# Kernel tuning notes

Hardware: AMD Instinct MI355X
Metric: run time of the kernel (lower is better)

The kernel has to match this reference:

```python
import jax, jax.numpy as jnp
import numpy as np

B, N, D = 2048, 256, 2
HID = 256
MU, SIGMA = 0.1, 0.2  # concrete drift/diffusion for the abstract SDE: dX = mu*X dt + sigma*X dW


def _init_lin(key, fan_in, fan_out):
    return jax.random.normal(key, (fan_in, fan_out), dtype=jnp.float32) / np.sqrt(fan_in)


def setup_inputs() -> dict:
    key = jax.random.key(0)
    ks = jax.random.split(key, 8)
    ts = jnp.linspace(0.0, 1.0, N, dtype=jnp.float32)
    x0 = jax.random.normal(ks[0], (B, D), dtype=jnp.float32)
    eps = jax.random.normal(ks[1], (B, N, D), dtype=jnp.float32)  # raw unit gaussians
    return {
        "ts": ts, "x0": x0, "eps": eps,
        "fW0": _init_lin(ks[2], D + 1, HID), "fb0": jnp.zeros((HID,), jnp.float32),
        "fW1": _init_lin(ks[3], HID, HID), "fb1": jnp.zeros((HID,), jnp.float32),
        "fW2": _init_lin(ks[4], HID, 1), "fb2": jnp.zeros((1,), jnp.float32),
        "gW0": _init_lin(ks[5], D + 1, HID), "gb0": jnp.zeros((HID,), jnp.float32),
        "gW1": _init_lin(ks[6], HID, HID), "gb1": jnp.zeros((HID,), jnp.float32),
        "gW2": _init_lin(ks[7], HID, D), "gb2": jnp.zeros((D,), jnp.float32),
    }


def _mlp(tx, params):
    h = tx
    n = len(params)
    for i, (W, b) in enumerate(params):
        h = h @ W + b
        if i < n - 1:
            h = jax.nn.relu(h)
    return h


def _final(x):
    # concrete terminal condition g(X_T) = ||X_T||^2 (BaseFinal stand-in)
    return jnp.sum(x * x, axis=-1, keepdims=True)


def reference(ts, x0, eps, fW0, fb0, fW1, fb1, fW2, fb2, gW0, gb0, gW1, gb1, gW2, gb2):
    dt = ts[1:] - ts[:-1]                                  # (N-1,)
    dW = eps[:, : N - 1, :] * jnp.sqrt(dt)[None, :, None]  # (B, N-1, D) scaled increments

    def step(x, inp):
        dw_t, h = inp                                      # dw_t: (B,D), h: scalar
        x_new = x + MU * x * h + SIGMA * x * dw_t
        return x_new, x_new

    _, traj = jax.lax.scan(step, x0, (jnp.transpose(dW, (1, 0, 2)), dt))
    x = jnp.concatenate([x0[:, None, :], jnp.transpose(traj, (1, 0, 2))], axis=1)  # (B,N,D)
    # last increment slot is never filled in the torch loop -> zeros
    dW_full = jnp.concatenate([dW, jnp.zeros((B, 1, D), dW.dtype)], axis=1)        # (B,N,D)

    final_value = _final(x[:, -1, :])                      # (B,1)
    t = jnp.broadcast_to(ts[None, :, None], (B, N, 1))
    tx = jnp.concatenate([t, x], axis=2)                   # (B,N,D+1)

    Y = _mlp(tx, [(fW0, fb0), (fW1, fb1), (fW2, fb2)])     # (B,N,1)
    Z = _mlp(tx, [(gW0, gb0), (gW1, gb1), (gW2, gb2)])     # (B,N,D)

    # per-step targets: Y_{t+1} detached, final_value at the last step
    targets = jnp.concatenate(
        [jax.lax.stop_gradient(Y[:, 1:, :]), final_value[:, None, :]], axis=1)
    preds = Y + jnp.sum(Z * dW_full, axis=2, keepdims=True)  # (B,N,1)
    # sum over time of per-step MSE (mean over batch)
    loss = jnp.sum(jnp.mean((preds - targets) ** 2, axis=(0, 2)))
    return loss, Y, final_value
```

## Files before the change

kernel.cpp:

```cpp
#include <hip/hip_runtime.h>
#include <math.h>

#define B_ 2048
#define N_ 256
#define R_ (B_*N_)
#define MU_ 0.1f
#define SIGMA_ 0.2f
#define TILE_M 64
#define GRID_MLP 512
#define ITERS (R_ / TILE_M / GRID_MLP)

typedef __attribute__((ext_vector_type(4))) float f32x4;
typedef __attribute__((ext_vector_type(4))) int   i32x4;
typedef __attribute__((ext_vector_type(8))) int   i32x8;

__global__ void prep_weights(const float* __restrict__ fW1, const float* __restrict__ gW1,
                             unsigned int* __restrict__ wswz) {
    int idx = blockIdx.x * 256 + threadIdx.x;
    if (idx >= 2 * 16384) return;
    int m = idx >> 14, wi = idx & 16383;
    int frag = wi >> 9;
    int lane = (wi >> 3) & 63, q = wi & 7;
    int ki = frag >> 4, ct = frag & 15;
    int k = ki * 128 + (lane >> 4) * 32 + q * 4;
    int c = ct * 16 + (lane & 15);
    const float* W = m ? gW1 : fW1;
    float v0 = W[(k + 0) * 256 + c];
    float v1 = W[(k + 1) * 256 + c];
    float v2 = W[(k + 2) * 256 + c];
    float v3 = W[(k + 3) * 256 + c];
    int u = __builtin_amdgcn_cvt_pk_fp8_f32(v0, v1, 0, false);
    u = __builtin_amdgcn_cvt_pk_fp8_f32(v2, v3, u, true);
    wswz[idx] = (unsigned int)u;
}

__global__ void traj_kernel(const float* __restrict__ ts, const float* __restrict__ x0,
                            const float* __restrict__ eps, float* __restrict__ xs,
                            float* __restrict__ fv) {
    int gid = blockIdx.x * 256 + threadIdx.x;
    int b = gid >> 6, lane = gid & 63;
    int n0 = lane * 4;

    float t0 = ts[n0], t1 = ts[n0 + 1], t2 = ts[n0 + 2], t3 = ts[n0 + 3];
    float t4 = (n0 + 4 < N_) ? ts[n0 + 4] : t3;
    float h0 = t1 - t0, h1 = t2 - t1, h2 = t3 - t2, h3 = t4 - t3;
    float s0 = sqrtf(h0), s1 = sqrtf(h1), s2 = sqrtf(h2), s3 = sqrtf(h3);

    const float4* e4 = (const float4*)(eps + (size_t)(b * N_ + n0) * 2);
    float4 ea = e4[0], eb = e4[1];
    float f0a = 1.f + MU_ * h0 + SIGMA_ * (ea.x * s0);
    float f0b = 1.f + MU_ * h0 + SIGMA_ * (ea.y * s0);
    float f1a = 1.f + MU_ * h1 + SIGMA_ * (ea.z * s1);
    float f1b = 1.f + MU_ * h1 + SIGMA_ * (ea.w * s1);
    float f2a = 1.f + MU_ * h2 + SIGMA_ * (eb.x * s2);
    float f2b = 1.f + MU_ * h2 + SIGMA_ * (eb.y * s2);
    float f3a = 1.f + MU_ * h3 + SIGMA_ * (eb.z * s3);
    float f3b = 1.f + MU_ * h3 + SIGMA_ * (eb.w * s3);

    float Pa = f0a * f1a * f2a * f3a;
    float Pb = f0b * f1b * f2b * f3b;
    float Sa = Pa, Sb = Pb;
#pragma unroll
    for (int d = 1; d < 64; d <<= 1) {
        float va = __shfl_up(Sa, d);
        float vb = __shfl_up(Sb, d);
        if (lane >= d) { Sa *= va; Sb *= vb; }
    }
    float Ea = __shfl_up(Sa, 1);
    float Eb = __shfl_up(Sb, 1);
    if (lane == 0) { Ea = 1.f; Eb = 1.f; }

    float x0a = x0[2 * b], x0b = x0[2 * b + 1];
    float xa0 = x0a * Ea, xb0 = x0b * Eb;
    float xa1 = xa0 * f0a, xb1 = xb0 * f0b;
    float xa2 = xa1 * f1a, xb2 = xb1 * f1b;
    float xa3 = xa2 * f2a, xb3 = xb2 * f2b;

    float4* xsv = (float4*)(xs + (size_t)(b * N_ + n0) * 2);
    xsv[0] = make_float4(xa0, xb0, xa1, xb1);
    xsv[1] = make_float4(xa2, xb2, xa3, xb3);
    if (lane == 63) fv[b] = xa3 * xa3 + xb3 * xb3;
}

__global__ __launch_bounds__(512) void mlp_kernel(
        const float* __restrict__ ts, const float* __restrict__ eps, const float* __restrict__ xs,
        const unsigned int* __restrict__ wswz,
        const float* __restrict__ fW0, const float* __restrict__ fb0,
        const float* __restrict__ fb1, const float* __restrict__ fW2, const float* __restrict__ fb2,
        const float* __restrict__ gW0, const float* __restrict__ gb0,
        const float* __restrict__ gb1, const float* __restrict__ gW2, const float* __restrict__ gb2,
        float* __restrict__ Yout, float* __restrict__ zdot) {

    __shared__ __align__(16) unsigned char h0s[2][TILE_M * 256];
    __shared__ float st[TILE_M * ITERS], sx1[TILE_M * ITERS], sx2[TILE_M * ITERS];
    __shared__ float sd0[TILE_M * ITERS], sd1[TILE_M * ITERS];
    __shared__ float red[2][8][TILE_M];

    const int MLP = blockIdx.x & 1;
    const int bid = blockIdx.x >> 1;

    const float* W0 = MLP ? gW0 : fW0;
    const float* b0 = MLP ? gb0 : fb0;
    const float* b1 = MLP ? gb1 : fb1;
    const float* W2 = MLP ? gW2 : fW2;
    const float* b2 = MLP ? gb2 : fb2;
    float* outp     = MLP ? zdot : Yout;

    const int tid  = threadIdx.x;
    const int lane = tid & 63;
    const int w    = tid >> 6;
    const int arow = lane & 15;
    const int rg   = lane >> 4;

    const int c0 = (tid & 63) * 4;
    const int row0 = (tid >> 6) * 8;
    f32x4 w0t = *(const f32x4*)(W0 + c0);
    f32x4 w0x = *(const f32x4*)(W0 + 256 + c0);
    f32x4 w0y = *(const f32x4*)(W0 + 512 + c0);
    f32x4 w0bv = *(const f32x4*)(b0 + c0);

    f32x4 bi0 = *(const f32x4*)(b1 + w * 32 + 4 * rg);
    f32x4 bi1 = *(const f32x4*)(b1 + w * 32 + 16 + 4 * rg);
    f32x4 w20v[2], w21v[2];
#pragma unroll
    for (int p = 0; p < 2; ++p) {
        int c = w * 32 + p * 16 + 4 * rg;
        if (MLP) {
            f32x4 lo = *(const f32x4*)(W2 + 2 * c);
            f32x4 hi = *(const f32x4*)(W2 + 2 * c + 4);
            w20v[p] = (f32x4){lo[0], lo[2], hi[0], hi[2]};
            w21v[p] = (f32x4){lo[1], lo[3], hi[1], hi[3]};
        } else {
            w20v[p] = *(const f32x4*)(W2 + c);
            w21v[p] = (f32x4){0.f, 0.f, 0.f, 0.f};
        }
    }
    const float b20 = b2[0];
    const float b21 = MLP ? b2[1] : 0.f;

    i32x8 afrag[2][2];
    {
        const i32x4* wsw4 = (const i32x4*)(wswz + MLP * 16384);
#pragma unroll
        for (int ki = 0; ki < 2; ++ki)
#pragma unroll
            for (int p = 0; p < 2; ++p) {
                int base = ((ki * 16 + (w * 2 + p)) * 64 + lane) * 2;
                i32x4 lo = wsw4[base], hi = wsw4[base + 1];
                afrag[ki][p] = __builtin_shufflevector(lo, hi, 0, 1, 2, 3, 4, 5, 6, 7);
            }
    }

#pragma unroll
    for (int q = 0; q < 2; ++q) {
        int s = q * 512 + tid;
        int it = s >> 6, i = s & 63;
        int r = (bid + it * GRID_MLP) * TILE_M + i;
        int n = r & (N_ - 1);
        float2 xv = ((const float2*)xs)[r];
        float tv = ts[n];
        st[s] = tv; sx1[s] = xv.x; sx2[s] = xv.y;
        if (MLP) {
            float sdt = (n < N_ - 1) ? sqrtf(ts[n + 1] - tv) : 0.f;
            float2 ev = ((const float2*)eps)[r];
            sd0[s] = ev.x * sdt; sd1[s] = ev.y * sdt;
        }
    }
    __syncthreads();

#pragma unroll
    for (int ii = 0; ii < 8; ++ii) {
        int r = row0 + ii;
        float t = st[r], x1 = sx1[r], x2 = sx2[r];
        f32x4 h;
#pragma unroll
        for (int j = 0; j < 4; ++j)
            h[j] = fmaxf(fmaf(t, w0t[j], fmaf(x1, w0x[j], fmaf(x2, w0y[j], w0bv[j]))), 0.f);
        int q = __builtin_amdgcn_cvt_pk_fp8_f32(h[0], h[1], 0, false);
        q = __builtin_amdgcn_cvt_pk_fp8_f32(h[2], h[3], q, true);
        int off = r * 256 + (c0 ^ ((r & 7) << 5));
        *(unsigned int*)(h0s[0] + off) = (unsigned int)q;
    }
    __syncthreads();

    for (int t = 0; t < ITERS; ++t) {
        const int sb = t & 1;

        if (t > 0 && tid < TILE_M) {
            const int pb = sb ^ 1;
            float s = red[pb][0][tid] + red[pb][1][tid] + red[pb][2][tid] + red[pb][3][tid]
                    + red[pb][4][tid] + red[pb][5][tid] + red[pb][6][tid] + red[pb][7][tid];
            if (!MLP) s += b20;
            outp[(bid + (t - 1) * GRID_MLP) * TILE_M + tid] = s;
        }

        f32x4 acc[4][2];
#pragma unroll
        for (int rt = 0; rt < 4; ++rt) { acc[rt][0] = bi0; acc[rt][1] = bi1; }
#pragma unroll
        for (int ki = 0; ki < 2; ++ki) {
#pragma unroll
            for (int rt = 0; rt < 4; ++rt) {
                int row = rt * 16 + arow;
                int roff = row * 256 + ((ki * 128 + rg * 32) ^ ((row & 7) << 5));
                i32x4 blo = *(const i32x4*)(h0s[sb] + roff);
                i32x4 bhi = *(const i32x4*)(h0s[sb] + roff + 16);
                i32x8 bf = __builtin_shufflevector(blo, bhi, 0, 1, 2, 3, 4, 5, 6, 7);
                acc[rt][0] = __builtin_amdgcn_mfma_scale_f32_16x16x128_f8f6f4(
                                 afrag[ki][0], bf, acc[rt][0], 0, 0, 0, 127, 0, 127);
                acc[rt][1] = __builtin_amdgcn_mfma_scale_f32_16x16x128_f8f6f4(
                                 afrag[ki][1], bf, acc[rt][1], 0, 0, 0, 127, 0, 127);
            }
        }

#pragma unroll
        for (int rt = 0; rt < 4; ++rt) {
            float A0 = 0.f, A1 = 0.f;
#pragma unroll
            for (int p = 0; p < 2; ++p) {
#pragma unroll
                for (int i = 0; i < 4; ++i) {
                    float v = fmaxf(acc[rt][p][i], 0.f);
                    A0 = fmaf(v, w20v[p][i], A0);
                    if (MLP) A1 = fmaf(v, w21v[p][i], A1);
                }
            }
            A0 += __shfl_xor(A0, 16); A0 += __shfl_xor(A0, 32);
            if (MLP) { A1 += __shfl_xor(A1, 16); A1 += __shfl_xor(A1, 32); }
            if (rg == 0) {
                int row = rt * 16 + arow;
                float rv;
                if (MLP) {
                    int s = t * TILE_M + row;
                    float d0 = sd0[s], d1 = sd1[s];
                    rv = fmaf(A1, d1, A0 * d0);
                    if (w == 0) rv += fmaf(b21, d1, b20 * d0);
                } else {
                    rv = A0;
                }
                red[sb][w][row] = rv;
            }
        }

        if (t + 1 < ITERS) {
            const int sbase = (t + 1) * TILE_M;
#pragma unroll
            for (int ii = 0; ii < 8; ++ii) {
                int r = row0 + ii;
                int s = sbase + r;
                float tv = st[s], x1 = sx1[s], x2 = sx2[s];
                f32x4 h;
#pragma unroll
                for (int j = 0; j < 4; ++j)
                    h[j] = fmaxf(fmaf(tv, w0t[j], fmaf(x1, w0x[j], fmaf(x2, w0y[j], w0bv[j]))), 0.f);
                int q = __builtin_amdgcn_cvt_pk_fp8_f32(h[0], h[1], 0, false);
                q = __builtin_amdgcn_cvt_pk_fp8_f32(h[2], h[3], q, true);
                int off = r * 256 + (c0 ^ ((r & 7) << 5));
                *(unsigned int*)(h0s[sb ^ 1] + off) = (unsigned int)q;
            }
        }
        __syncthreads();
    }
    if (tid < TILE_M) {
        const int pb = (ITERS - 1) & 1;
        float s = red[pb][0][tid] + red[pb][1][tid] + red[pb][2][tid] + red[pb][3][tid]
                + red[pb][4][tid] + red[pb][5][tid] + red[pb][6][tid] + red[pb][7][tid];
        if (!MLP) s += b20;
        outp[(bid + (ITERS - 1) * GRID_MLP) * TILE_M + tid] = s;
    }
}

__global__ void loss_partial_kernel(const float* __restrict__ Yout, const float* __restrict__ fv,
                                    const float* __restrict__ zdot, float* __restrict__ partials) {
    __shared__ float wred[4];
    int tid = threadIdx.x;
    float s = 0.f;
    for (int r = blockIdx.x * 256 + tid; r < R_; r += gridDim.x * 256) {
        int n = r & (N_ - 1);
        float pred = Yout[r] + zdot[r];
        float target = (n == N_ - 1) ? fv[r >> 8] : Yout[r + 1];
        float d = pred - target;
        s = fmaf(d, d, s);
    }
#pragma unroll
    for (int m = 1; m < 64; m <<= 1) s += __shfl_xor(s, m);
    if ((tid & 63) == 0) wred[tid >> 6] = s;
    __syncthreads();
    if (tid == 0) partials[blockIdx.x] = wred[0] + wred[1] + wred[2] + wred[3];
}

__global__ void loss_final_kernel(const float* __restrict__ partials, float* __restrict__ out) {
    __shared__ float wred[4];
    int tid = threadIdx.x;
    float s = partials[tid] + partials[256 + tid] + partials[512 + tid] + partials[768 + tid];
#pragma unroll
    for (int m = 1; m < 64; m <<= 1) s += __shfl_xor(s, m);
    if ((tid & 63) == 0) wred[tid >> 6] = s;
    __syncthreads();
    if (tid == 0) out[0] = (wred[0] + wred[1] + wred[2] + wred[3]) * (1.0f / B_);
}

extern "C" void kernel_launch(void* const* d_in, const int* in_sizes, int n_in,
                              void* d_out, int out_size, void* d_ws, size_t ws_size,
                              hipStream_t stream) {
    const float* ts  = (const float*)d_in[0];
    const float* x0  = (const float*)d_in[1];
    const float* eps = (const float*)d_in[2];
    const float* fW0 = (const float*)d_in[3];
    const float* fb0 = (const float*)d_in[4];
    const float* fW1 = (const float*)d_in[5];
    const float* fb1 = (const float*)d_in[6];
    const float* fW2 = (const float*)d_in[7];
    const float* fb2 = (const float*)d_in[8];
    const float* gW0 = (const float*)d_in[9];
    const float* gb0 = (const float*)d_in[10];
    const float* gW1 = (const float*)d_in[11];
    const float* gb1 = (const float*)d_in[12];
    const float* gW2 = (const float*)d_in[13];
    const float* gb2 = (const float*)d_in[14];

    float* out  = (float*)d_out;
    float* Yout = out + 1;
    float* fv   = out + 1 + R_;

    char* wsb = (char*)d_ws;
    float* xs           = (float*)wsb;
    unsigned int* wswz  = (unsigned int*)(wsb + (4 << 20));
    float* zdot         = (float*)(wsb + (4 << 20) + (256 << 10));
    float* partials     = (float*)(wsb + (4 << 20) + (256 << 10) + (2 << 20));

    hipLaunchKernelGGL(prep_weights, dim3(128), dim3(256), 0, stream, fW1, gW1, wswz);
    hipLaunchKernelGGL(traj_kernel, dim3(512), dim3(256), 0, stream, ts, x0, eps, xs, fv);
    hipLaunchKernelGGL(mlp_kernel, dim3(2 * GRID_MLP), dim3(512), 0, stream,
                       ts, eps, xs, wswz,
                       fW0, fb0, fb1, fW2, fb2,
                       gW0, gb0, gb1, gW2, gb2, Yout, zdot);
    hipLaunchKernelGGL(loss_partial_kernel, dim3(1024), dim3(256), 0, stream, Yout, fv, zdot, partials);
    hipLaunchKernelGGL(loss_final_kernel, dim3(1), dim3(256), 0, stream, partials, out);
}
```

Measured before the change: 174.8 us.

## Rework MLP kernel LDS layout: 8-byte swizzle, packed inputs, shuffle-free reduction

Changes the fp8 activation tile swizzle to an 8-byte granularity XOR over 16 rows and reads B fragments as four 8-byte LDS loads, aiming to reduce bank conflicts. Packs the t/x and dW staging arrays into float4/float2 structs so each row is fetched in one vector load. Replaces the cross-lane shuffle reduction with per-lane partial writes into a padded 32-wide reduction buffer that is summed with vector reads. Adds s_setprio around the MFMA loop. The trade-offs are more LDS instructions per fragment and a larger reduction buffer, which may affect occupancy.

```diff
diff --git a/kernel.cpp b/kernel.cpp
--- a/kernel.cpp
+++ b/kernel.cpp
@@ -11,7 +11,7 @@
 #define ITERS (R_ / TILE_M / GRID_MLP)
 
 typedef __attribute__((ext_vector_type(4))) float f32x4;
-typedef __attribute__((ext_vector_type(4))) int   i32x4;
+typedef __attribute__((ext_vector_type(2))) int   i32x2;
 typedef __attribute__((ext_vector_type(8))) int   i32x8;
 
 __global__ void prep_weights(const float* __restrict__ fW1, const float* __restrict__ gW1,
@@ -92,9 +92,9 @@
         float* __restrict__ Yout, float* __restrict__ zdot) {
 
     __shared__ __align__(16) unsigned char h0s[2][TILE_M * 256];
-    __shared__ float st[TILE_M * ITERS], sx1[TILE_M * ITERS], sx2[TILE_M * ITERS];
-    __shared__ float sd0[TILE_M * ITERS], sd1[TILE_M * ITERS];
-    __shared__ float red[2][8][TILE_M];
+    __shared__ __align__(16) float4 sfx[TILE_M * ITERS];
+    __shared__ __align__(16) float2 sd[TILE_M * ITERS];
+    __shared__ __align__(16) float red2[2][TILE_M][36];
 
     const int MLP = blockIdx.x & 1;
     const int bid = blockIdx.x >> 1;
@@ -140,14 +140,14 @@
 
     i32x8 afrag[2][2];
     {
-        const i32x4* wsw4 = (const i32x4*)(wswz + MLP * 16384);
+        const i32x2* wsw2 = (const i32x2*)(wswz + MLP * 16384);
 #pragma unroll
         for (int ki = 0; ki < 2; ++ki)
 #pragma unroll
             for (int p = 0; p < 2; ++p) {
-                int base = ((ki * 16 + (w * 2 + p)) * 64 + lane) * 2;
-                i32x4 lo = wsw4[base], hi = wsw4[base + 1];
-                afrag[ki][p] = __builtin_shufflevector(lo, hi, 0, 1, 2, 3, 4, 5, 6, 7);
+                int base = ((ki * 16 + (w * 2 + p)) * 64 + lane) * 4;
+                i32x2 a0 = wsw2[base], a1 = wsw2[base + 1], a2 = wsw2[base + 2], a3 = wsw2[base + 3];
+                afrag[ki][p] = (i32x8){a0[0], a0[1], a1[0], a1[1], a2[0], a2[1], a3[0], a3[1]};
             }
     }
 
@@ -159,11 +159,11 @@
         int n = r & (N_ - 1);
         float2 xv = ((const float2*)xs)[r];
         float tv = ts[n];
-        st[s] = tv; sx1[s] = xv.x; sx2[s] = xv.y;
+        sfx[s] = make_float4(tv, xv.x, xv.y, 0.f);
         if (MLP) {
             float sdt = (n < N_ - 1) ? sqrtf(ts[n + 1] - tv) : 0.f;
             float2 ev = ((const float2*)eps)[r];
-            sd0[s] = ev.x * sdt; sd1[s] = ev.y * sdt;
+            sd[s] = make_float2(ev.x * sdt, ev.y * sdt);
         }
     }
     __syncthreads();
@@ -171,14 +171,14 @@
 #pragma unroll
     for (int ii = 0; ii < 8; ++ii) {
         int r = row0 + ii;
-        float t = st[r], x1 = sx1[r], x2 = sx2[r];
+        float4 v = sfx[r];
         f32x4 h;
 #pragma unroll
         for (int j = 0; j < 4; ++j)
-            h[j] = fmaxf(fmaf(t, w0t[j], fmaf(x1, w0x[j], fmaf(x2, w0y[j], w0bv[j]))), 0.f);
+            h[j] = fmaxf(fmaf(v.x, w0t[j], fmaf(v.y, w0x[j], fmaf(v.z, w0y[j], w0bv[j]))), 0.f);
         int q = __builtin_amdgcn_cvt_pk_fp8_f32(h[0], h[1], 0, false);
         q = __builtin_amdgcn_cvt_pk_fp8_f32(h[2], h[3], q, true);
-        int off = r * 256 + (c0 ^ ((r & 7) << 5));
+        int off = r * 256 + (c0 ^ ((r & 15) << 3));
         *(unsigned int*)(h0s[0] + off) = (unsigned int)q;
     }
     __syncthreads();
@@ -188,8 +188,13 @@
 
         if (t > 0 && tid < TILE_M) {
             const int pb = sb ^ 1;
-            float s = red[pb][0][tid] + red[pb][1][tid] + red[pb][2][tid] + red[pb][3][tid]
-                    + red[pb][4][tid] + red[pb][5][tid] + red[pb][6][tid] + red[pb][7][tid];
+            const float* rr = red2[pb][tid];
+            float s = 0.f;
+#pragma unroll
+            for (int j = 0; j < 32; j += 4) {
+                f32x4 v = *(const f32x4*)(rr + j);
+                s += (v[0] + v[1]) + (v[2] + v[3]);
+            }
             if (!MLP) s += b20;
             outp[(bid + (t - 1) * GRID_MLP) * TILE_M + tid] = s;
         }
@@ -197,21 +202,27 @@
         f32x4 acc[4][2];
 #pragma unroll
         for (int rt = 0; rt < 4; ++rt) { acc[rt][0] = bi0; acc[rt][1] = bi1; }
+        __builtin_amdgcn_s_setprio(1);
 #pragma unroll
         for (int ki = 0; ki < 2; ++ki) {
 #pragma unroll
             for (int rt = 0; rt < 4; ++rt) {
                 int row = rt * 16 + arow;
-                int roff = row * 256 + ((ki * 128 + rg * 32) ^ ((row & 7) << 5));
-                i32x4 blo = *(const i32x4*)(h0s[sb] + roff);
-                i32x4 bhi = *(const i32x4*)(h0s[sb] + roff + 16);
-                i32x8 bf = __builtin_shufflevector(blo, bhi, 0, 1, 2, 3, 4, 5, 6, 7);
+                const int rsw = (row & 15) << 3;
+                const unsigned char* bp = h0s[sb] + row * 256;
+                const int kb = ki * 128 + rg * 32;
+                i32x2 q0 = *(const i32x2*)(bp + ((kb +  0) ^ rsw));
+                i32x2 q1 = *(const i32x2*)(bp + ((kb +  8) ^ rsw));
+                i32x2 q2 = *(const i32x2*)(bp + ((kb + 16) ^ rsw));
+                i32x2 q3 = *(const i32x2*)(bp + ((kb + 24) ^ rsw));
+                i32x8 bf = (i32x8){q0[0], q0[1], q1[0], q1[1], q2[0], q2[1], q3[0], q3[1]};
                 acc[rt][0] = __builtin_amdgcn_mfma_scale_f32_16x16x128_f8f6f4(
                                  afrag[ki][0], bf, acc[rt][0], 0, 0, 0, 127, 0, 127);
                 acc[rt][1] = __builtin_amdgcn_mfma_scale_f32_16x16x128_f8f6f4(
                                  afrag[ki][1], bf, acc[rt][1], 0, 0, 0, 127, 0, 127);
             }
         }
+        __builtin_amdgcn_s_setprio(0);
 
 #pragma unroll
         for (int rt = 0; rt < 4; ++rt) {
@@ -225,21 +236,16 @@
                     if (MLP) A1 = fmaf(v, w21v[p][i], A1);
                 }
             }
-            A0 += __shfl_xor(A0, 16); A0 += __shfl_xor(A0, 32);
-            if (MLP) { A1 += __shfl_xor(A1, 16); A1 += __shfl_xor(A1, 32); }
-            if (rg == 0) {
-                int row = rt * 16 + arow;
-                float rv;
-                if (MLP) {
-                    int s = t * TILE_M + row;
-                    float d0 = sd0[s], d1 = sd1[s];
-                    rv = fmaf(A1, d1, A0 * d0);
-                    if (w == 0) rv += fmaf(b21, d1, b20 * d0);
-                } else {
-                    rv = A0;
-                }
-                red[sb][w][row] = rv;
-            }
+            int row = rt * 16 + arow;
+            float rv;
+            if (MLP) {
+                float2 dv = sd[t * TILE_M + row];
+                rv = fmaf(A1, dv.y, A0 * dv.x);
+                if (w == 0) rv += fmaf(b21, dv.y, b20 * dv.x);
+            } else {
+                rv = A0;
+            }
+            red2[sb][row][w * 4 + rg] = rv;
         }
 
         if (t + 1 < ITERS) {
@@ -247,15 +253,14 @@
 #pragma unroll
             for (int ii = 0; ii < 8; ++ii) {
                 int r = row0 + ii;
-                int s = sbase + r;
-                float tv = st[s], x1 = sx1[s], x2 = sx2[s];
+                float4 v = sfx[sbase + r];
                 f32x4 h;
 #pragma unroll
                 for (int j = 0; j < 4; ++j)
-                    h[j] = fmaxf(fmaf(tv, w0t[j], fmaf(x1, w0x[j], fmaf(x2, w0y[j], w0bv[j]))), 0.f);
+                    h[j] = fmaxf(fmaf(v.x, w0t[j], fmaf(v.y, w0x[j], fmaf(v.z, w0y[j], w0bv[j]))), 0.f);
                 int q = __builtin_amdgcn_cvt_pk_fp8_f32(h[0], h[1], 0, false);
                 q = __builtin_amdgcn_cvt_pk_fp8_f32(h[2], h[3], q, true);
-                int off = r * 256 + (c0 ^ ((r & 7) << 5));
+                int off = r * 256 + (c0 ^ ((r & 15) << 3));
                 *(unsigned int*)(h0s[sb ^ 1] + off) = (unsigned int)q;
             }
         }
@@ -263,8 +268,13 @@
     }
     if (tid < TILE_M) {
         const int pb = (ITERS - 1) & 1;
-        float s = red[pb][0][tid] + red[pb][1][tid] + red[pb][2][tid] + red[pb][3][tid]
-                + red[pb][4][tid] + red[pb][5][tid] + red[pb][6][tid] + red[pb][7][tid];
+        const float* rr = red2[pb][tid];
+        float s = 0.f;
+#pragma unroll
+        for (int j = 0; j < 32; j += 4) {
+            f32x4 v = *(const f32x4*)(rr + j);
+            s += (v[0] + v[1]) + (v[2] + v[3]);
+        }
         if (!MLP) s += b20;
         outp[(bid + (ITERS - 1) * GRID_MLP) * TILE_M + tid] = s;
     }
```

Result: faster. 154.4 us, median of 2 (-11.6%).
